# Optimization experiments

Measured on AMD Instinct MI355X. Metric: run time of the kernel, lower is better.

Reference implementation:

```python
import jax, jax.numpy as jnp
import numpy as np

N_NODES = 50000
N_EDGES = 1600000
IN_FEATS = 128
HIDDEN = 128
NUM_CLASSES = 40


def setup_inputs() -> dict:
    key = jax.random.key(0)
    k1, k2, k3, k4, k5 = jax.random.split(key, 5)
    features = jax.random.normal(k1, (N_NODES, IN_FEATS), dtype=jnp.float32)
    src = jax.random.randint(k2, (N_EDGES,), 0, N_NODES, dtype=jnp.int32)
    dst = jax.random.randint(k3, (N_EDGES,), 0, N_NODES, dtype=jnp.int32)
    W1 = jax.random.normal(k4, (IN_FEATS, HIDDEN), dtype=jnp.float32) / np.sqrt(IN_FEATS)
    b1 = jnp.zeros((HIDDEN,), dtype=jnp.float32)
    W2 = jax.random.normal(k5, (HIDDEN, NUM_CLASSES), dtype=jnp.float32) / np.sqrt(HIDDEN)
    b2 = jnp.zeros((NUM_CLASSES,), dtype=jnp.float32)
    return {"features": features, "src": src, "dst": dst,
            "W1": W1, "b1": b1, "W2": W2, "b2": b2}


def _degree_norms(src, dst, n_nodes):
    ones = jnp.ones(src.shape[0], dtype=jnp.float32)
    deg_out = jax.ops.segment_sum(ones, src, num_segments=n_nodes)
    deg_in = jax.ops.segment_sum(ones, dst, num_segments=n_nodes)
    # DGL GraphConv clamps degree at 1 (zero-degree nodes get norm 1)
    norm_src = jax.lax.rsqrt(jnp.maximum(deg_out, 1.0))
    norm_dst = jax.lax.rsqrt(jnp.maximum(deg_in, 1.0))
    return norm_src, norm_dst


def _graph_conv(x, W, b, src, dst, norm_src, norm_dst, n_nodes):
    # norm='both': h = D_in^{-1/2} A^T (D_out^{-1/2} x W) + b
    h = (x * norm_src[:, None]) @ W          # [N, out]
    msgs = h[src]                             # gather  [E, out]
    agg = jax.ops.segment_sum(msgs, dst, num_segments=n_nodes)  # scatter-add [N, out]
    return agg * norm_dst[:, None] + b


def reference(features, src, dst, W1, b1, W2, b2):
    n = features.shape[0]
    norm_src, norm_dst = _degree_norms(src, dst, n)
    h = jax.nn.relu(_graph_conv(features, W1, b1, src, dst, norm_src, norm_dst, n))
    h = _graph_conv(h, W2, b2, src, dst, norm_src, norm_dst, n)
    return h
```

## Files before the change

kernel.cpp:

```cpp
#include <hip/hip_runtime.h>


#define CHUNK 16384
#define CHUNK_SHIFT 14
#define NSLICES 64

typedef int iv4 __attribute__((ext_vector_type(4)));
typedef short short8 __attribute__((ext_vector_type(8)));
typedef float f32x4 __attribute__((ext_vector_type(4)));

__device__ __forceinline__ unsigned f2bf_bits(float f) {
    unsigned u = __float_as_uint(f);
    return (u + 0x7FFFu + ((u >> 16) & 1u)) >> 16;
}
__device__ __forceinline__ unsigned pack_bf2(float a, float b) {
    return f2bf_bits(a) | (f2bf_bits(b) << 16);
}
__device__ __forceinline__ float bflo(unsigned v) { return __uint_as_float(v << 16); }
__device__ __forceinline__ float bfhi(unsigned v) { return __uint_as_float(v & 0xFFFF0000u); }


__global__ __launch_bounds__(256) void count_kernel(const int* __restrict__ src, const int* __restrict__ dst,
                                                    unsigned int* __restrict__ part, int E, int per) {
    __shared__ unsigned int h[CHUNK];
    int c = blockIdx.y, s = blockIdx.x, t = threadIdx.x;
    #pragma unroll
    for (int i = 0; i < CHUNK / 256; ++i) h[i * 256 + t] = 0;
    __syncthreads();
    int base = c << CHUNK_SHIFT;
    int beg = s * per;
    int end = min(E, beg + per);
    int nv = (end - beg) >> 2;
    const iv4* d4 = (const iv4*)(dst + beg);
    const iv4* s4 = (const iv4*)(src + beg);
    for (int i = t; i < nv; i += 256) {
        iv4 dv = __builtin_nontemporal_load(d4 + i);
        iv4 sv = __builtin_nontemporal_load(s4 + i);
        int x;
        x = dv.x - base; if ((unsigned)x < CHUNK) atomicAdd(&h[x], 1u);
        x = dv.y - base; if ((unsigned)x < CHUNK) atomicAdd(&h[x], 1u);
        x = dv.z - base; if ((unsigned)x < CHUNK) atomicAdd(&h[x], 1u);
        x = dv.w - base; if ((unsigned)x < CHUNK) atomicAdd(&h[x], 1u);
        x = sv.x - base; if ((unsigned)x < CHUNK) atomicAdd(&h[x], 0x10000u);
        x = sv.y - base; if ((unsigned)x < CHUNK) atomicAdd(&h[x], 0x10000u);
        x = sv.z - base; if ((unsigned)x < CHUNK) atomicAdd(&h[x], 0x10000u);
        x = sv.w - base; if ((unsigned)x < CHUNK) atomicAdd(&h[x], 0x10000u);
    }
    for (int e = beg + (nv << 2) + t; e < end; e += 256) {
        int x = dst[e] - base; if ((unsigned)x < CHUNK) atomicAdd(&h[x], 1u);
        x = src[e] - base;     if ((unsigned)x < CHUNK) atomicAdd(&h[x], 0x10000u);
    }
    __syncthreads();
    unsigned int* out = part + (((size_t)(c * NSLICES + s)) << CHUNK_SHIFT);
    #pragma unroll
    for (int i = 0; i < CHUNK / 256; ++i) __builtin_nontemporal_store(h[i * 256 + t], out + i * 256 + t);
}

__global__ __launch_bounds__(256) void reduce_kernel(const unsigned int* __restrict__ part,
                                                     float* __restrict__ norm_src, float* __restrict__ norm_dst,
                                                     int* __restrict__ deg_dst_i, int N) {
    int d = blockIdx.x * 256 + threadIdx.x;
    if (d >= N) return;
    int c = d >> CHUNK_SHIFT, idx = d & (CHUNK - 1);
    const unsigned int* p = part + (((size_t)c * NSLICES) << CHUNK_SHIFT) + idx;
    unsigned int dsum = 0, ssum = 0;
    #pragma unroll
    for (int s = 0; s < NSLICES; ++s) {
        unsigned int v = __builtin_nontemporal_load(p + ((size_t)s << CHUNK_SHIFT));
        dsum += v & 0xFFFFu;
        ssum += v >> 16;
    }
    deg_dst_i[d] = (int)dsum;
    norm_src[d] = rsqrtf(fmaxf((float)ssum, 1.0f));
    norm_dst[d] = rsqrtf(fmaxf((float)dsum, 1.0f));
}

__global__ __launch_bounds__(256) void scanA_kernel(const int* __restrict__ deg, int* __restrict__ bsum, int N) {
    __shared__ int wsum[4];
    int b = blockIdx.x, t = threadIdx.x, lane = t & 63, wid = t >> 6;
    int i0 = b * 1024 + t * 4;
    int s = 0;
    if (i0 + 3 < N) {
        int4 v = *(const int4*)(deg + i0);
        s = v.x + v.y + v.z + v.w;
    } else {
        for (int k = 0; k < 4; ++k) { int i = i0 + k; if (i < N) s += deg[i]; }
    }
    #pragma unroll
    for (int off = 32; off; off >>= 1) s += __shfl_down(s, off, 64);
    if (lane == 0) wsum[wid] = s;
    __syncthreads();
    if (t == 0) bsum[b] = wsum[0] + wsum[1] + wsum[2] + wsum[3];
}

__global__ __launch_bounds__(64) void scanB_kernel(int* __restrict__ bsum, int NB,
                                                   int* __restrict__ row_ptr, int N) {
    int t = threadIdx.x;
    int v = (t < NB) ? bsum[t] : 0;
    int x = v;
    #pragma unroll
    for (int off = 1; off < 64; off <<= 1) {
        int y = __shfl_up(x, off, 64);
        if (t >= off) x += y;
    }
    if (t < NB) bsum[t] = x - v;
    if (t == 63) row_ptr[N] = x;
}

__global__ __launch_bounds__(256) void scanC_kernel(const int* __restrict__ deg, const int* __restrict__ bsum,
                                                    int* __restrict__ row_ptr, int N) {
    __shared__ int wsum[4];
    int b = blockIdx.x, t = threadIdx.x, lane = t & 63, wid = t >> 6;
    int i0 = b * 1024 + t * 4;
    int4 v = make_int4(0, 0, 0, 0);
    if (i0 + 3 < N) v = *(const int4*)(deg + i0);
    else {
        v.x = (i0 < N) ? deg[i0] : 0;
        v.y = (i0 + 1 < N) ? deg[i0 + 1] : 0;
        v.z = (i0 + 2 < N) ? deg[i0 + 2] : 0;
        v.w = (i0 + 3 < N) ? deg[i0 + 3] : 0;
    }
    int tsum = v.x + v.y + v.z + v.w;
    int x = tsum;
    #pragma unroll
    for (int off = 1; off < 64; off <<= 1) {
        int y = __shfl_up(x, off, 64);
        if (lane >= off) x += y;
    }
    if (lane == 63) wsum[wid] = x;
    __syncthreads();
    int woff = 0;
    for (int k = 0; k < wid; ++k) woff += wsum[k];
    int base = bsum[b] + woff + (x - tsum);
    int e0 = base, e1 = e0 + v.x, e2 = e1 + v.y, e3 = e2 + v.z;
    if (i0 + 3 < N) *(int4*)(row_ptr + i0) = make_int4(e0, e1, e2, e3);
    else {
        if (i0 < N) row_ptr[i0] = e0;
        if (i0 + 1 < N) row_ptr[i0 + 1] = e1;
        if (i0 + 2 < N) row_ptr[i0 + 2] = e2;
        if (i0 + 3 < N) row_ptr[i0 + 3] = e3;
    }
}

__global__ __launch_bounds__(256) void offsets_kernel(unsigned int* __restrict__ part,
                                                      const int* __restrict__ row_ptr, int N) {
    int d = blockIdx.x * 256 + threadIdx.x;
    if (d >= N) return;
    int c = d >> CHUNK_SHIFT, idx = d & (CHUNK - 1);
    unsigned int* p = part + (((size_t)c * NSLICES) << CHUNK_SHIFT) + idx;
    unsigned int running = (unsigned int)row_ptr[d];
    #pragma unroll
    for (int s = 0; s < NSLICES; ++s) {
        unsigned int v = __builtin_nontemporal_load(p + ((size_t)s << CHUNK_SHIFT));
        __builtin_nontemporal_store(running, p + ((size_t)s << CHUNK_SHIFT));
        running += v & 0xFFFFu;
    }
}

__global__ __launch_bounds__(256) void scatter_kernel(const int* __restrict__ src, const int* __restrict__ dst,
                                                      const unsigned int* __restrict__ cum,
                                                      int* __restrict__ col, int E, int per) {
    __shared__ int cur[CHUNK];
    int c = blockIdx.y, s = blockIdx.x, t = threadIdx.x;
    const unsigned int* cc = cum + (((size_t)(c * NSLICES + s)) << CHUNK_SHIFT);
    #pragma unroll
    for (int i = 0; i < CHUNK / 256; ++i) cur[i * 256 + t] = (int)__builtin_nontemporal_load(cc + i * 256 + t);
    __syncthreads();
    int base = c << CHUNK_SHIFT;
    int beg = s * per;
    int end = min(E, beg + per);
    int nv = (end - beg) >> 2;
    const iv4* d4 = (const iv4*)(dst + beg);
    const iv4* s4 = (const iv4*)(src + beg);
    for (int i = t; i < nv; i += 256) {
        iv4 dv = __builtin_nontemporal_load(d4 + i);
        iv4 sv = __builtin_nontemporal_load(s4 + i);
        int x;
        x = dv.x - base; if ((unsigned)x < CHUNK) col[atomicAdd(&cur[x], 1)] = sv.x;
        x = dv.y - base; if ((unsigned)x < CHUNK) col[atomicAdd(&cur[x], 1)] = sv.y;
        x = dv.z - base; if ((unsigned)x < CHUNK) col[atomicAdd(&cur[x], 1)] = sv.z;
        x = dv.w - base; if ((unsigned)x < CHUNK) col[atomicAdd(&cur[x], 1)] = sv.w;
    }
    for (int e = beg + (nv << 2) + t; e < end; e += 256) {
        int x = dst[e] - base;
        if ((unsigned)x < CHUNK) col[atomicAdd(&cur[x], 1)] = src[e];
    }
}


__global__ __launch_bounds__(256) void wprep_kernel(const float* __restrict__ W, unsigned short* __restrict__ wt) {
    int tid = blockIdx.x * 256 + threadIdx.x;
    int c = tid & 127, kg = tid >> 7;
    unsigned p[4];
    #pragma unroll
    for (int j = 0; j < 4; ++j) {
        float v0 = W[(kg * 8 + 2 * j) * 128 + c];
        float v1 = W[(kg * 8 + 2 * j + 1) * 128 + c];
        p[j] = pack_bf2(v0, v1);
    }
    *(uint4*)(wt + (size_t)c * 128 + kg * 8) = make_uint4(p[0], p[1], p[2], p[3]);
}

__global__ __launch_bounds__(256) void wprep2_kernel(const float* __restrict__ W2, unsigned short* __restrict__ wt2) {
    int tid = blockIdx.x * 256 + threadIdx.x;
    int c = tid >> 4, kg = tid & 15;
    unsigned p[4];
    #pragma unroll
    for (int j = 0; j < 4; ++j) {
        float v0 = (c < 40) ? W2[(kg * 8 + 2 * j) * 40 + c] : 0.f;
        float v1 = (c < 40) ? W2[(kg * 8 + 2 * j + 1) * 40 + c] : 0.f;
        p[j] = pack_bf2(v0, v1);
    }
    *(uint4*)(wt2 + (size_t)c * 128 + kg * 8) = make_uint4(p[0], p[1], p[2], p[3]);
}

__global__ __launch_bounds__(256) void gemm1_kernel(const float* __restrict__ x, const float* __restrict__ norm,
                                                    const unsigned short* __restrict__ wt,
                                                    unsigned short* __restrict__ h1u, int N) {
    __shared__ uint4 xs4[1024];
    char* xsb = (char*)xs4;
    int t = threadIdx.x;
    int rb = blockIdx.x * 64;
    #pragma unroll
    for (int i = 0; i < 8; ++i) {
        int idx = i * 256 + t;
        int row = idx >> 5, k4 = (idx & 31) << 2;
        int gr = rb + row;
        float4 v = make_float4(0.f, 0.f, 0.f, 0.f);
        if (gr < N) {
            v = *(const float4*)(x + (size_t)gr * 128 + k4);
            float nm = norm[gr];
            v.x *= nm; v.y *= nm; v.z *= nm; v.w *= nm;
        }
        int boff = row * 256 + ((k4 * 2) ^ ((row & 7) << 4));
        *(uint2*)(xsb + boff) = make_uint2(pack_bf2(v.x, v.y), pack_bf2(v.z, v.w));
    }
    __syncthreads();
    int w = t >> 6, lane = t & 63;
    int lrow = lane & 15, g = lane >> 4;
    int sw = (lrow & 7) << 4;
    int rloc = (w << 4) + lrow;
    short8 a[4];
    #pragma unroll
    for (int kt = 0; kt < 4; ++kt)
        a[kt] = *(const short8*)(xsb + rloc * 256 + ((kt * 64 + g * 16) ^ sw));
    f32x4 acc[8];
    #pragma unroll
    for (int ct = 0; ct < 8; ++ct) acc[ct] = (f32x4){0.f, 0.f, 0.f, 0.f};
    #pragma unroll
    for (int ct = 0; ct < 8; ++ct) {
        const unsigned short* wb = wt + (size_t)(ct * 16 + lrow) * 128 + g * 8;
        short8 b0 = *(const short8*)(wb);
        short8 b1 = *(const short8*)(wb + 32);
        short8 b2 = *(const short8*)(wb + 64);
        short8 b3 = *(const short8*)(wb + 96);
        acc[ct] = __builtin_amdgcn_mfma_f32_16x16x32_bf16(a[0], b0, acc[ct], 0, 0, 0);
        acc[ct] = __builtin_amdgcn_mfma_f32_16x16x32_bf16(a[1], b1, acc[ct], 0, 0, 0);
        acc[ct] = __builtin_amdgcn_mfma_f32_16x16x32_bf16(a[2], b2, acc[ct], 0, 0, 0);
        acc[ct] = __builtin_amdgcn_mfma_f32_16x16x32_bf16(a[3], b3, acc[ct], 0, 0, 0);
    }
    int rbase = rb + (w << 4) + g * 4;
    #pragma unroll
    for (int reg = 0; reg < 4; ++reg) {
        int rowg = rbase + reg;
        if (rowg < N) {
            #pragma unroll
            for (int ct = 0; ct < 8; ++ct)
                h1u[(size_t)rowg * 128 + ct * 16 + lrow] = (unsigned short)f2bf_bits(acc[ct][reg]);
        }
    }
}

__global__ __launch_bounds__(256) void gemmW2_kernel(const unsigned short* __restrict__ yu,
                                                     const unsigned short* __restrict__ wt2,
                                                     unsigned short* __restrict__ wu, int N) {
    __shared__ uint4 xs4[1024];
    char* xsb = (char*)xs4;
    int t = threadIdx.x;
    int rb = blockIdx.x * 64;
    #pragma unroll
    for (int i = 0; i < 8; ++i) {
        int idx = i * 256 + t;
        int row = idx >> 5, q = idx & 31;
        int gr = rb + row;
        uint2 v = make_uint2(0u, 0u);
        if (gr < N) v = *(const uint2*)(yu + (size_t)gr * 128 + q * 4);
        int boff = row * 256 + ((q * 8) ^ ((row & 7) << 4));
        *(uint2*)(xsb + boff) = v;
    }
    __syncthreads();
    int w = t >> 6, lane = t & 63;
    int lrow = lane & 15, g = lane >> 4;
    int sw = (lrow & 7) << 4;
    int rloc = (w << 4) + lrow;
    short8 a[4];
    #pragma unroll
    for (int kt = 0; kt < 4; ++kt)
        a[kt] = *(const short8*)(xsb + rloc * 256 + ((kt * 64 + g * 16) ^ sw));
    f32x4 acc[3];
    #pragma unroll
    for (int ct = 0; ct < 3; ++ct) acc[ct] = (f32x4){0.f, 0.f, 0.f, 0.f};
    #pragma unroll
    for (int ct = 0; ct < 3; ++ct) {
        const unsigned short* wb = wt2 + (size_t)(ct * 16 + lrow) * 128 + g * 8;
        short8 b0 = *(const short8*)(wb);
        short8 b1 = *(const short8*)(wb + 32);
        short8 b2 = *(const short8*)(wb + 64);
        short8 b3 = *(const short8*)(wb + 96);
        acc[ct] = __builtin_amdgcn_mfma_f32_16x16x32_bf16(a[0], b0, acc[ct], 0, 0, 0);
        acc[ct] = __builtin_amdgcn_mfma_f32_16x16x32_bf16(a[1], b1, acc[ct], 0, 0, 0);
        acc[ct] = __builtin_amdgcn_mfma_f32_16x16x32_bf16(a[2], b2, acc[ct], 0, 0, 0);
        acc[ct] = __builtin_amdgcn_mfma_f32_16x16x32_bf16(a[3], b3, acc[ct], 0, 0, 0);
    }
    int rbase = rb + (w << 4) + g * 4;
    #pragma unroll
    for (int reg = 0; reg < 4; ++reg) {
        int rowg = rbase + reg;
        if (rowg < N) {
            #pragma unroll
            for (int ct = 0; ct < 3; ++ct)
                wu[(size_t)rowg * 64 + ct * 16 + lrow] = (unsigned short)f2bf_bits(acc[ct][reg]);
            wu[(size_t)rowg * 64 + 48 + lrow] = 0;
        }
    }
}


#define ACC8(v)  { a0 += bflo(v.x); a1 += bfhi(v.x); a2 += bflo(v.y); a3 += bfhi(v.y); \
                   a4 += bflo(v.z); a5 += bfhi(v.z); a6 += bflo(v.w); a7 += bfhi(v.w); }

__global__ __launch_bounds__(256) void agg1_kernel(const int* __restrict__ row_ptr, const int* __restrict__ col,
                                                   const uint4* __restrict__ h1q, const float* __restrict__ norm_dst,
                                                   const float* __restrict__ norm_src,
                                                   const float* __restrict__ b1, uint4* __restrict__ yq, int N) {
    int t = threadIdx.x;
    int wid = t >> 6, lane = t & 63;
    int g = lane >> 4, f = lane & 15;
    int n = blockIdx.x * 4 + wid;
    if (n >= N) return;
    int beg = row_ptr[n], deg = row_ptr[n + 1] - beg;
    const int* cp = col + beg;
    float a0 = 0, a1 = 0, a2 = 0, a3 = 0, a4 = 0, a5 = 0, a6 = 0, a7 = 0;
    int e = 0;
    for (; e + 16 <= deg; e += 16) {
        int s0 = cp[e + g];
        int s1 = cp[e + 4 + g];
        int s2 = cp[e + 8 + g];
        int s3 = cp[e + 12 + g];
        uint4 v0 = h1q[(size_t)s0 * 16 + f];
        uint4 v1 = h1q[(size_t)s1 * 16 + f];
        uint4 v2 = h1q[(size_t)s2 * 16 + f];
        uint4 v3 = h1q[(size_t)s3 * 16 + f];
        ACC8(v0); ACC8(v1); ACC8(v2); ACC8(v3);
    }
    for (; e < deg; e += 4) {
        int idx = e + g;
        if (idx < deg) {
            uint4 v = h1q[(size_t)cp[idx] * 16 + f];
            ACC8(v);
        }
    }
    a0 += __shfl_xor(a0, 16, 64); a0 += __shfl_xor(a0, 32, 64);
    a1 += __shfl_xor(a1, 16, 64); a1 += __shfl_xor(a1, 32, 64);
    a2 += __shfl_xor(a2, 16, 64); a2 += __shfl_xor(a2, 32, 64);
    a3 += __shfl_xor(a3, 16, 64); a3 += __shfl_xor(a3, 32, 64);
    a4 += __shfl_xor(a4, 16, 64); a4 += __shfl_xor(a4, 32, 64);
    a5 += __shfl_xor(a5, 16, 64); a5 += __shfl_xor(a5, 32, 64);
    a6 += __shfl_xor(a6, 16, 64); a6 += __shfl_xor(a6, 32, 64);
    a7 += __shfl_xor(a7, 16, 64); a7 += __shfl_xor(a7, 32, 64);
    if (g == 0) {
        float nd = norm_dst[n];
        float ns = norm_src[n];
        float4 bA = *(const float4*)(b1 + f * 8);
        float4 bB = *(const float4*)(b1 + f * 8 + 4);
        float o0 = ns * fmaxf(a0 * nd + bA.x, 0.f);
        float o1 = ns * fmaxf(a1 * nd + bA.y, 0.f);
        float o2 = ns * fmaxf(a2 * nd + bA.z, 0.f);
        float o3 = ns * fmaxf(a3 * nd + bA.w, 0.f);
        float o4 = ns * fmaxf(a4 * nd + bB.x, 0.f);
        float o5 = ns * fmaxf(a5 * nd + bB.y, 0.f);
        float o6 = ns * fmaxf(a6 * nd + bB.z, 0.f);
        float o7 = ns * fmaxf(a7 * nd + bB.w, 0.f);
        uint4 p;
        p.x = pack_bf2(o0, o1); p.y = pack_bf2(o2, o3);
        p.z = pack_bf2(o4, o5); p.w = pack_bf2(o6, o7);
        yq[(size_t)n * 16 + f] = p;
    }
}

__global__ __launch_bounds__(256) void aggZ_kernel(const int* __restrict__ row_ptr, const int* __restrict__ col,
                                                   const uint4* __restrict__ wq, const float* __restrict__ norm_dst,
                                                   const float* __restrict__ b2, float* __restrict__ out, int N) {
    int t = threadIdx.x;
    int wid = t >> 6, lane = t & 63;
    int g = lane >> 3, f = lane & 7;
    int n = blockIdx.x * 4 + wid;
    if (n >= N) return;
    int beg = row_ptr[n], deg = row_ptr[n + 1] - beg;
    const int* cp = col + beg;
    float a0 = 0, a1 = 0, a2 = 0, a3 = 0, a4 = 0, a5 = 0, a6 = 0, a7 = 0;
    int e = 0;
    for (; e + 32 <= deg; e += 32) {
        int s0 = cp[e + g];
        int s1 = cp[e + 8 + g];
        int s2 = cp[e + 16 + g];
        int s3 = cp[e + 24 + g];
        uint4 v0 = wq[(size_t)s0 * 8 + f];
        uint4 v1 = wq[(size_t)s1 * 8 + f];
        uint4 v2 = wq[(size_t)s2 * 8 + f];
        uint4 v3 = wq[(size_t)s3 * 8 + f];
        ACC8(v0); ACC8(v1); ACC8(v2); ACC8(v3);
    }
    for (; e < deg; e += 8) {
        int idx = e + g;
        if (idx < deg) {
            uint4 v = wq[(size_t)cp[idx] * 8 + f];
            ACC8(v);
        }
    }
    a0 += __shfl_xor(a0, 8, 64); a0 += __shfl_xor(a0, 16, 64); a0 += __shfl_xor(a0, 32, 64);
    a1 += __shfl_xor(a1, 8, 64); a1 += __shfl_xor(a1, 16, 64); a1 += __shfl_xor(a1, 32, 64);
    a2 += __shfl_xor(a2, 8, 64); a2 += __shfl_xor(a2, 16, 64); a2 += __shfl_xor(a2, 32, 64);
    a3 += __shfl_xor(a3, 8, 64); a3 += __shfl_xor(a3, 16, 64); a3 += __shfl_xor(a3, 32, 64);
    a4 += __shfl_xor(a4, 8, 64); a4 += __shfl_xor(a4, 16, 64); a4 += __shfl_xor(a4, 32, 64);
    a5 += __shfl_xor(a5, 8, 64); a5 += __shfl_xor(a5, 16, 64); a5 += __shfl_xor(a5, 32, 64);
    a6 += __shfl_xor(a6, 8, 64); a6 += __shfl_xor(a6, 16, 64); a6 += __shfl_xor(a6, 32, 64);
    a7 += __shfl_xor(a7, 8, 64); a7 += __shfl_xor(a7, 16, 64); a7 += __shfl_xor(a7, 32, 64);
    if (g == 0 && f < 5) {
        float nd = norm_dst[n];
        int j0 = f * 8;
        float4 bA = *(const float4*)(b2 + j0);
        float4 bB = *(const float4*)(b2 + j0 + 4);
        float* op = out + (size_t)n * 40 + j0;
        *(float4*)(op)     = make_float4(a0 * nd + bA.x, a1 * nd + bA.y, a2 * nd + bA.z, a3 * nd + bA.w);
        *(float4*)(op + 4) = make_float4(a4 * nd + bB.x, a5 * nd + bB.y, a6 * nd + bB.z, a7 * nd + bB.w);
    }
}

extern "C" void kernel_launch(void* const* d_in, const int* in_sizes, int n_in,
                              void* d_out, int out_size, void* d_ws, size_t ws_size,
                              hipStream_t stream) {
    const float* x  = (const float*)d_in[0];
    const int* src  = (const int*)d_in[1];
    const int* dst  = (const int*)d_in[2];
    const float* W1 = (const float*)d_in[3];
    const float* b1 = (const float*)d_in[4];
    const float* W2 = (const float*)d_in[5];
    const float* b2 = (const float*)d_in[6];
    float* out = (float*)d_out;

    int N = in_sizes[0] / 128;
    int E = in_sizes[1];
    int NPAD = (N + 63) & ~63;
    int NCHUNKS = (N + CHUNK - 1) >> CHUNK_SHIFT;
    int per = ((E + NSLICES - 1) / NSLICES + 3) & ~3;
    int NB = (N + 1023) / 1024;

    float* ws = (float*)d_ws;
    float* norm_src = ws;
    float* norm_dst = ws + NPAD;
    int* deg_dst_i  = (int*)(ws + 2 * (size_t)NPAD);
    int* row_ptr    = (int*)(ws + 3 * (size_t)NPAD);
    int* bsum       = (int*)(ws + 4 * (size_t)NPAD);
    unsigned short* wt1 = (unsigned short*)(ws + 4 * (size_t)NPAD + 64);
    unsigned short* wt2 = (unsigned short*)(ws + 4 * (size_t)NPAD + 64 + 8192);
    int* col        = (int*)(ws + 4 * (size_t)NPAD + 64 + 8192 + 3072);
    size_t h1_off   = ((size_t)4 * NPAD + 64 + 8192 + 3072 + E + 15) & ~(size_t)15;
    unsigned short* h1u = (unsigned short*)(ws + h1_off);
    uint4* h1q      = (uint4*)h1u;
    unsigned short* yu = h1u + (size_t)NPAD * 128;
    uint4* yq       = (uint4*)yu;
    unsigned short* wu = h1u;
    uint4* wq       = (uint4*)wu;
    unsigned int* part = (unsigned int*)h1u;

    dim3 cgrid(NSLICES, NCHUNKS);
    wprep_kernel<<<8, 256, 0, stream>>>(W1, wt1);
    wprep2_kernel<<<3, 256, 0, stream>>>(W2, wt2);
    count_kernel<<<cgrid, 256, 0, stream>>>(src, dst, part, E, per);
    reduce_kernel<<<(N + 255) / 256, 256, 0, stream>>>(part, norm_src, norm_dst, deg_dst_i, N);
    scanA_kernel<<<NB, 256, 0, stream>>>(deg_dst_i, bsum, N);
    scanB_kernel<<<1, 64, 0, stream>>>(bsum, NB, row_ptr, N);
    scanC_kernel<<<NB, 256, 0, stream>>>(deg_dst_i, bsum, row_ptr, N);
    offsets_kernel<<<(N + 255) / 256, 256, 0, stream>>>(part, row_ptr, N);
    scatter_kernel<<<cgrid, 256, 0, stream>>>(src, dst, part, col, E, per);
    gemm1_kernel<<<(N + 63) / 64, 256, 0, stream>>>(x, norm_src, wt1, h1u, N);
    agg1_kernel<<<(N + 3) / 4, 256, 0, stream>>>(row_ptr, col, h1q, norm_dst, norm_src, b1, yq, N);
    gemmW2_kernel<<<(N + 63) / 64, 256, 0, stream>>>(yu, wt2, wu, N);
    aggZ_kernel<<<(N + 3) / 4, 256, 0, stream>>>(row_ptr, col, wq, norm_dst, b2, out, N);
}
```

Before: 207.4 us.

## Fuse degree scan into reduce/offsets kernels, merge weight prep, shrink layer-2 rows

The degree reduction now also produces per-block sums, and the scan's final pass is merged into the offsets kernel, cutting the CSR build from five launches to three. The two weight-prep kernels are combined into one launch. The layer-2 intermediate is stored with a 40-column bf16 stride instead of a padded 64-column one, so the aggregation gathers five 16-byte vectors per row instead of eight, with lanes f>=5 left idle. Block sums now cover 256 nodes each, so the single-block scan must handle up to 256 entries, which sets a ceiling on N.

```diff
diff --git a/kernel.cpp b/kernel.cpp
--- a/kernel.cpp
+++ b/kernel.cpp
@@ -58,34 +58,25 @@
 
 __global__ __launch_bounds__(256) void reduce_kernel(const unsigned int* __restrict__ part,
                                                      float* __restrict__ norm_src, float* __restrict__ norm_dst,
-                                                     int* __restrict__ deg_dst_i, int N) {
-    int d = blockIdx.x * 256 + threadIdx.x;
-    if (d >= N) return;
-    int c = d >> CHUNK_SHIFT, idx = d & (CHUNK - 1);
-    const unsigned int* p = part + (((size_t)c * NSLICES) << CHUNK_SHIFT) + idx;
-    unsigned int dsum = 0, ssum = 0;
-    #pragma unroll
-    for (int s = 0; s < NSLICES; ++s) {
-        unsigned int v = __builtin_nontemporal_load(p + ((size_t)s << CHUNK_SHIFT));
-        dsum += v & 0xFFFFu;
-        ssum += v >> 16;
-    }
-    deg_dst_i[d] = (int)dsum;
-    norm_src[d] = rsqrtf(fmaxf((float)ssum, 1.0f));
-    norm_dst[d] = rsqrtf(fmaxf((float)dsum, 1.0f));
-}
-
-__global__ __launch_bounds__(256) void scanA_kernel(const int* __restrict__ deg, int* __restrict__ bsum, int N) {
+                                                     int* __restrict__ deg_dst_i, int* __restrict__ bsum, int N) {
     __shared__ int wsum[4];
     int b = blockIdx.x, t = threadIdx.x, lane = t & 63, wid = t >> 6;
-    int i0 = b * 1024 + t * 4;
-    int s = 0;
-    if (i0 + 3 < N) {
-        int4 v = *(const int4*)(deg + i0);
-        s = v.x + v.y + v.z + v.w;
-    } else {
-        for (int k = 0; k < 4; ++k) { int i = i0 + k; if (i < N) s += deg[i]; }
-    }
+    int d = b * 256 + t;
+    unsigned int dsum = 0, ssum = 0;
+    if (d < N) {
+        int c = d >> CHUNK_SHIFT, idx = d & (CHUNK - 1);
+        const unsigned int* p = part + (((size_t)c * NSLICES) << CHUNK_SHIFT) + idx;
+        #pragma unroll
+        for (int s = 0; s < NSLICES; ++s) {
+            unsigned int v = __builtin_nontemporal_load(p + ((size_t)s << CHUNK_SHIFT));
+            dsum += v & 0xFFFFu;
+            ssum += v >> 16;
+        }
+        deg_dst_i[d] = (int)dsum;
+        norm_src[d] = rsqrtf(fmaxf((float)ssum, 1.0f));
+        norm_dst[d] = rsqrtf(fmaxf((float)dsum, 1.0f));
+    }
+    int s = (int)dsum;
     #pragma unroll
     for (int off = 32; off; off >>= 1) s += __shfl_down(s, off, 64);
     if (lane == 0) wsum[wid] = s;
@@ -93,35 +84,12 @@
     if (t == 0) bsum[b] = wsum[0] + wsum[1] + wsum[2] + wsum[3];
 }
 
-__global__ __launch_bounds__(64) void scanB_kernel(int* __restrict__ bsum, int NB,
-                                                   int* __restrict__ row_ptr, int N) {
-    int t = threadIdx.x;
+__global__ __launch_bounds__(256) void scanB_kernel(int* __restrict__ bsum, int NB,
+                                                    int* __restrict__ row_ptr, int N) {
+    __shared__ int wsum[4];
+    int t = threadIdx.x, lane = t & 63, wid = t >> 6;
     int v = (t < NB) ? bsum[t] : 0;
     int x = v;
-    #pragma unroll
-    for (int off = 1; off < 64; off <<= 1) {
-        int y = __shfl_up(x, off, 64);
-        if (t >= off) x += y;
-    }
-    if (t < NB) bsum[t] = x - v;
-    if (t == 63) row_ptr[N] = x;
-}
-
-__global__ __launch_bounds__(256) void scanC_kernel(const int* __restrict__ deg, const int* __restrict__ bsum,
-                                                    int* __restrict__ row_ptr, int N) {
-    __shared__ int wsum[4];
-    int b = blockIdx.x, t = threadIdx.x, lane = t & 63, wid = t >> 6;
-    int i0 = b * 1024 + t * 4;
-    int4 v = make_int4(0, 0, 0, 0);
-    if (i0 + 3 < N) v = *(const int4*)(deg + i0);
-    else {
-        v.x = (i0 < N) ? deg[i0] : 0;
-        v.y = (i0 + 1 < N) ? deg[i0 + 1] : 0;
-        v.z = (i0 + 2 < N) ? deg[i0 + 2] : 0;
-        v.w = (i0 + 3 < N) ? deg[i0 + 3] : 0;
-    }
-    int tsum = v.x + v.y + v.z + v.w;
-    int x = tsum;
     #pragma unroll
     for (int off = 1; off < 64; off <<= 1) {
         int y = __shfl_up(x, off, 64);
@@ -131,29 +99,39 @@
     __syncthreads();
     int woff = 0;
     for (int k = 0; k < wid; ++k) woff += wsum[k];
-    int base = bsum[b] + woff + (x - tsum);
-    int e0 = base, e1 = e0 + v.x, e2 = e1 + v.y, e3 = e2 + v.z;
-    if (i0 + 3 < N) *(int4*)(row_ptr + i0) = make_int4(e0, e1, e2, e3);
-    else {
-        if (i0 < N) row_ptr[i0] = e0;
-        if (i0 + 1 < N) row_ptr[i0 + 1] = e1;
-        if (i0 + 2 < N) row_ptr[i0 + 2] = e2;
-        if (i0 + 3 < N) row_ptr[i0 + 3] = e3;
-    }
+    if (t < NB) bsum[t] = woff + x - v;
+    if (t == 255) row_ptr[N] = woff + x;
 }
 
 __global__ __launch_bounds__(256) void offsets_kernel(unsigned int* __restrict__ part,
-                                                      const int* __restrict__ row_ptr, int N) {
-    int d = blockIdx.x * 256 + threadIdx.x;
-    if (d >= N) return;
-    int c = d >> CHUNK_SHIFT, idx = d & (CHUNK - 1);
-    unsigned int* p = part + (((size_t)c * NSLICES) << CHUNK_SHIFT) + idx;
-    unsigned int running = (unsigned int)row_ptr[d];
-    #pragma unroll
-    for (int s = 0; s < NSLICES; ++s) {
-        unsigned int v = __builtin_nontemporal_load(p + ((size_t)s << CHUNK_SHIFT));
-        __builtin_nontemporal_store(running, p + ((size_t)s << CHUNK_SHIFT));
-        running += v & 0xFFFFu;
+                                                      const int* __restrict__ deg, const int* __restrict__ bsum,
+                                                      int* __restrict__ row_ptr, int N) {
+    __shared__ int wsum[4];
+    int b = blockIdx.x, t = threadIdx.x, lane = t & 63, wid = t >> 6;
+    int d = b * 256 + t;
+    int v = (d < N) ? deg[d] : 0;
+    int x = v;
+    #pragma unroll
+    for (int off = 1; off < 64; off <<= 1) {
+        int y = __shfl_up(x, off, 64);
+        if (lane >= off) x += y;
+    }
+    if (lane == 63) wsum[wid] = x;
+    __syncthreads();
+    int woff = 0;
+    for (int k = 0; k < wid; ++k) woff += wsum[k];
+    int excl = bsum[b] + woff + (x - v);
+    if (d < N) {
+        row_ptr[d] = excl;
+        int c = d >> CHUNK_SHIFT, idx = d & (CHUNK - 1);
+        unsigned int* p = part + (((size_t)c * NSLICES) << CHUNK_SHIFT) + idx;
+        unsigned int running = (unsigned int)excl;
+        #pragma unroll
+        for (int s = 0; s < NSLICES; ++s) {
+            unsigned int pv = __builtin_nontemporal_load(p + ((size_t)s << CHUNK_SHIFT));
+            __builtin_nontemporal_store(running, p + ((size_t)s << CHUNK_SHIFT));
+            running += pv & 0xFFFFu;
+        }
     }
 }
 
@@ -188,30 +166,32 @@
 }
 
 
-__global__ __launch_bounds__(256) void wprep_kernel(const float* __restrict__ W, unsigned short* __restrict__ wt) {
-    int tid = blockIdx.x * 256 + threadIdx.x;
-    int c = tid & 127, kg = tid >> 7;
-    unsigned p[4];
-    #pragma unroll
-    for (int j = 0; j < 4; ++j) {
-        float v0 = W[(kg * 8 + 2 * j) * 128 + c];
-        float v1 = W[(kg * 8 + 2 * j + 1) * 128 + c];
-        p[j] = pack_bf2(v0, v1);
-    }
-    *(uint4*)(wt + (size_t)c * 128 + kg * 8) = make_uint4(p[0], p[1], p[2], p[3]);
-}
-
-__global__ __launch_bounds__(256) void wprep2_kernel(const float* __restrict__ W2, unsigned short* __restrict__ wt2) {
-    int tid = blockIdx.x * 256 + threadIdx.x;
-    int c = tid >> 4, kg = tid & 15;
-    unsigned p[4];
-    #pragma unroll
-    for (int j = 0; j < 4; ++j) {
-        float v0 = (c < 40) ? W2[(kg * 8 + 2 * j) * 40 + c] : 0.f;
-        float v1 = (c < 40) ? W2[(kg * 8 + 2 * j + 1) * 40 + c] : 0.f;
-        p[j] = pack_bf2(v0, v1);
-    }
-    *(uint4*)(wt2 + (size_t)c * 128 + kg * 8) = make_uint4(p[0], p[1], p[2], p[3]);
+__global__ __launch_bounds__(256) void wprep_kernel(const float* __restrict__ W1, unsigned short* __restrict__ wt1,
+                                                    const float* __restrict__ W2, unsigned short* __restrict__ wt2) {
+    int bid = blockIdx.x;
+    if (bid < 8) {
+        int tid = bid * 256 + threadIdx.x;
+        int c = tid & 127, kg = tid >> 7;
+        unsigned p[4];
+        #pragma unroll
+        for (int j = 0; j < 4; ++j) {
+            float v0 = W1[(kg * 8 + 2 * j) * 128 + c];
+            float v1 = W1[(kg * 8 + 2 * j + 1) * 128 + c];
+            p[j] = pack_bf2(v0, v1);
+        }
+        *(uint4*)(wt1 + (size_t)c * 128 + kg * 8) = make_uint4(p[0], p[1], p[2], p[3]);
+    } else {
+        int tid = (bid - 8) * 256 + threadIdx.x;
+        int c = tid >> 4, kg = tid & 15;
+        unsigned p[4];
+        #pragma unroll
+        for (int j = 0; j < 4; ++j) {
+            float v0 = (c < 40) ? W2[(kg * 8 + 2 * j) * 40 + c] : 0.f;
+            float v1 = (c < 40) ? W2[(kg * 8 + 2 * j + 1) * 40 + c] : 0.f;
+            p[j] = pack_bf2(v0, v1);
+        }
+        *(uint4*)(wt2 + (size_t)c * 128 + kg * 8) = make_uint4(p[0], p[1], p[2], p[3]);
+    }
 }
 
 __global__ __launch_bounds__(256) void gemm1_kernel(const float* __restrict__ x, const float* __restrict__ norm,
@@ -318,9 +298,10 @@
         int rowg = rbase + reg;
         if (rowg < N) {
             #pragma unroll
-            for (int ct = 0; ct < 3; ++ct)
-                wu[(size_t)rowg * 64 + ct * 16 + lrow] = (unsigned short)f2bf_bits(acc[ct][reg]);
-            wu[(size_t)rowg * 64 + 48 + lrow] = 0;
+            for (int ct = 0; ct < 3; ++ct) {
+                int c = ct * 16 + lrow;
+                if (c < 40) wu[(size_t)rowg * 40 + c] = (unsigned short)f2bf_bits(acc[ct][reg]);
+            }
         }
     }
 }
@@ -394,6 +375,7 @@
     int t = threadIdx.x;
     int wid = t >> 6, lane = t & 63;
     int g = lane >> 3, f = lane & 7;
+    bool act = f < 5;
     int n = blockIdx.x * 4 + wid;
     if (n >= N) return;
     int beg = row_ptr[n], deg = row_ptr[n + 1] - beg;
@@ -405,16 +387,18 @@
         int s1 = cp[e + 8 + g];
         int s2 = cp[e + 16 + g];
         int s3 = cp[e + 24 + g];
-        uint4 v0 = wq[(size_t)s0 * 8 + f];
-        uint4 v1 = wq[(size_t)s1 * 8 + f];
-        uint4 v2 = wq[(size_t)s2 * 8 + f];
-        uint4 v3 = wq[(size_t)s3 * 8 + f];
-        ACC8(v0); ACC8(v1); ACC8(v2); ACC8(v3);
+        if (act) {
+            uint4 v0 = wq[(size_t)s0 * 5 + f];
+            uint4 v1 = wq[(size_t)s1 * 5 + f];
+            uint4 v2 = wq[(size_t)s2 * 5 + f];
+            uint4 v3 = wq[(size_t)s3 * 5 + f];
+            ACC8(v0); ACC8(v1); ACC8(v2); ACC8(v3);
+        }
     }
     for (; e < deg; e += 8) {
         int idx = e + g;
-        if (idx < deg) {
-            uint4 v = wq[(size_t)cp[idx] * 8 + f];
+        if (idx < deg && act) {
+            uint4 v = wq[(size_t)cp[idx] * 5 + f];
             ACC8(v);
         }
     }
@@ -426,7 +410,7 @@
     a5 += __shfl_xor(a5, 8, 64); a5 += __shfl_xor(a5, 16, 64); a5 += __shfl_xor(a5, 32, 64);
     a6 += __shfl_xor(a6, 8, 64); a6 += __shfl_xor(a6, 16, 64); a6 += __shfl_xor(a6, 32, 64);
     a7 += __shfl_xor(a7, 8, 64); a7 += __shfl_xor(a7, 16, 64); a7 += __shfl_xor(a7, 32, 64);
-    if (g == 0 && f < 5) {
+    if (g == 0 && act) {
         float nd = norm_dst[n];
         int j0 = f * 8;
         float4 bA = *(const float4*)(b2 + j0);
@@ -454,7 +438,7 @@
     int NPAD = (N + 63) & ~63;
     int NCHUNKS = (N + CHUNK - 1) >> CHUNK_SHIFT;
     int per = ((E + NSLICES - 1) / NSLICES + 3) & ~3;
-    int NB = (N + 1023) / 1024;
+    int NB = (N + 255) / 256;
 
     float* ws = (float*)d_ws;
     float* norm_src = ws;
@@ -462,10 +446,10 @@
     int* deg_dst_i  = (int*)(ws + 2 * (size_t)NPAD);
     int* row_ptr    = (int*)(ws + 3 * (size_t)NPAD);
     int* bsum       = (int*)(ws + 4 * (size_t)NPAD);
-    unsigned short* wt1 = (unsigned short*)(ws + 4 * (size_t)NPAD + 64);
-    unsigned short* wt2 = (unsigned short*)(ws + 4 * (size_t)NPAD + 64 + 8192);
-    int* col        = (int*)(ws + 4 * (size_t)NPAD + 64 + 8192 + 3072);
-    size_t h1_off   = ((size_t)4 * NPAD + 64 + 8192 + 3072 + E + 15) & ~(size_t)15;
+    unsigned short* wt1 = (unsigned short*)(ws + 4 * (size_t)NPAD + 256);
+    unsigned short* wt2 = (unsigned short*)(ws + 4 * (size_t)NPAD + 256 + 8192);
+    int* col        = (int*)(ws + 4 * (size_t)NPAD + 256 + 8192 + 3072);
+    size_t h1_off   = ((size_t)4 * NPAD + 256 + 8192 + 3072 + E + 15) & ~(size_t)15;
     unsigned short* h1u = (unsigned short*)(ws + h1_off);
     uint4* h1q      = (uint4*)h1u;
     unsigned short* yu = h1u + (size_t)NPAD * 128;
@@ -475,14 +459,11 @@
     unsigned int* part = (unsigned int*)h1u;
 
     dim3 cgrid(NSLICES, NCHUNKS);
-    wprep_kernel<<<8, 256, 0, stream>>>(W1, wt1);
-    wprep2_kernel<<<3, 256, 0, stream>>>(W2, wt2);
+    wprep_kernel<<<11, 256, 0, stream>>>(W1, wt1, W2, wt2);
     count_kernel<<<cgrid, 256, 0, stream>>>(src, dst, part, E, per);
-    reduce_kernel<<<(N + 255) / 256, 256, 0, stream>>>(part, norm_src, norm_dst, deg_dst_i, N);
-    scanA_kernel<<<NB, 256, 0, stream>>>(deg_dst_i, bsum, N);
-    scanB_kernel<<<1, 64, 0, stream>>>(bsum, NB, row_ptr, N);
-    scanC_kernel<<<NB, 256, 0, stream>>>(deg_dst_i, bsum, row_ptr, N);
-    offsets_kernel<<<(N + 255) / 256, 256, 0, stream>>>(part, row_ptr, N);
+    reduce_kernel<<<NB, 256, 0, stream>>>(part, norm_src, norm_dst, deg_dst_i, bsum, N);
+    scanB_kernel<<<1, 256, 0, stream>>>(bsum, NB, row_ptr, N);
+    offsets_kernel<<<NB, 256, 0, stream>>>(part, deg_dst_i, bsum, row_ptr, N);
     scatter_kernel<<<cgrid, 256, 0, stream>>>(src, dst, part, col, E, per);
     gemm1_kernel<<<(N + 63) / 64, 256, 0, stream>>>(x, norm_src, wt1, h1u, N);
     agg1_kernel<<<(N + 3) / 4, 256, 0, stream>>>(row_ptr, col, h1q, norm_dst, norm_src, b1, yq, N);
```

Result: faster. 199.2 us (-3.9%).
